# Optimization experiments

Measured on AMD Instinct MI355X. Metric: run time of the kernel, lower is better.

## Reference

```python
import jax, jax.numpy as jnp
import numpy as np

B, T, I, H = 32, 512, 512, 512


def setup_inputs() -> dict:
    key = jax.random.key(0)
    k1, k2, k3, k4, k5 = jax.random.split(key, 5)
    s = 1.0 / np.sqrt(H)
    return {
        "x": jax.random.normal(k1, (B, T, I), dtype=jnp.float32),
        "Wx": jax.random.normal(k2, (4 * H, I), dtype=jnp.float32) * s,
        "bx": jax.random.normal(k3, (4 * H,), dtype=jnp.float32) * s,
        "Wh": jax.random.normal(k4, (4 * H, H), dtype=jnp.float32) * s,
        "bh": jax.random.normal(k5, (4 * H,), dtype=jnp.float32) * s,
    }


def _cell(gx, h, c, Wh, bh):
    # gx: [B, 4H] precomputed x2h contribution (incl. bx)
    gates = gx + h @ Wh.T + bh
    i_g, f_g, g_g, o_g = jnp.split(gates, 4, axis=1)  # torch chunk order
    i_t = jax.nn.sigmoid(i_g)
    f_t = jax.nn.sigmoid(f_g)
    g_t = jnp.tanh(g_g)
    o_t = jax.nn.sigmoid(o_g)
    cy = c * f_t + i_t * g_t
    hy = o_t * jnp.tanh(cy)
    return hy, cy


def reference(x, Wx, bx, Wh, bh):
    b, t, _ = x.shape
    hdim = Wh.shape[1]
    # Precompute input-to-hidden for all timesteps: [T, B, 4H]
    gx = (jnp.einsum('bti,gi->btg', x, Wx) + bx).transpose(1, 0, 2)
    gx_rev = gx[::-1]  # backward direction reads input[:, -t-1, :]

    h0 = jnp.zeros((b, hdim), dtype=x.dtype)
    carry0 = (h0, h0, h0, h0)  # hf, cf, hb, cb

    def step(carry, inp):
        hf, cf, hb, cb = carry
        gxf, gxb = inp
        hf, cf = _cell(gxf, hf, cf, Wh, bh)
        hb, cb = _cell(gxb, hb, cb, Wh, bh)
        return (hf, cf, hb, cb), (hf, hb)

    _, (out_f, out_b) = jax.lax.scan(step, carry0, (gx, gx_rev))
    # Faithful to original: backward outputs stacked in processing order (no flip)
    out = jnp.concatenate([out_f.transpose(1, 0, 2), out_b.transpose(1, 0, 2)], axis=2)
    return out
```

## Files before the change

kernel.cpp:

```cpp
#include <hip/hip_runtime.h>
#include <stdint.h>

typedef unsigned short ushort_t;
typedef float f32x4 __attribute__((ext_vector_type(4)));
typedef short short8 __attribute__((ext_vector_type(8)));

#define B_ 32
#define T_ 512
#define I_ 512
#define H_ 512
#define G_ 2048

__device__ __forceinline__ ushort_t f2bf(float f) {
    uint32_t u = __float_as_uint(f);
    u += 0x7FFFu + ((u >> 16) & 1u);
    return (ushort_t)(u >> 16);
}
__device__ __forceinline__ float bf2f(ushort_t s) {
    return __uint_as_float(((uint32_t)s) << 16);
}
__device__ __forceinline__ float sigm(float x) { return 1.0f / (1.0f + __expf(-x)); }
__device__ __forceinline__ float tanhx(float x) {
    float e = __expf(-2.0f * fabsf(x));
    float t = (1.0f - e) / (1.0f + e);
    return x >= 0.0f ? t : -t;
}

__global__ __launch_bounds__(256) void kcast(const float* __restrict__ in,
                                             ushort_t* __restrict__ out, int n4) {
    int i = blockIdx.x * 256 + threadIdx.x;
    if (i < n4) {
        float4 v = ((const float4*)in)[i];
        ushort4 o;
        o.x = f2bf(v.x); o.y = f2bf(v.y); o.z = f2bf(v.z); o.w = f2bf(v.w);
        ((ushort4*)out)[i] = o;
    }
}

__global__ __launch_bounds__(256) void kbias(const float* __restrict__ bx,
                                             const float* __restrict__ bh,
                                             float* __restrict__ bias) {
    int i = blockIdx.x * 256 + threadIdx.x;
    if (i < G_) bias[i] = bx[i] + bh[i];
}

__global__ __launch_bounds__(256, 2) void kgemm(const ushort_t* __restrict__ A,
                                                const ushort_t* __restrict__ Bm,
                                                const float* __restrict__ bias,
                                                ushort_t* __restrict__ C) {
    __shared__ __align__(16) ushort_t LA[4096];
    __shared__ __align__(16) ushort_t LB[4096];
    const int tid = threadIdx.x;
    const int lane = tid & 63, w = tid >> 6;
    const int quad = lane >> 4, l16 = lane & 15;
    const int bn = blockIdx.x, bm = blockIdx.y;
    const int wr = w >> 1, wc = w & 1;

    f32x4 acc[4][4] = {};

    for (int kt = 0; kt < 16; ++kt) {
#pragma unroll
        for (int r = 0; r < 2; ++r) {
            int o = r * 256 + tid;
            int m = o >> 2, slot = o & 3;
            int kc = slot ^ ((m >> 1) & 3);
            const ushort_t* ga = A  + (size_t)(bm * 128 + m) * I_ + kt * 32 + kc * 8;
            const ushort_t* gb = Bm + (size_t)(bn * 128 + m) * I_ + kt * 32 + kc * 8;
            __builtin_amdgcn_global_load_lds(
                (const __attribute__((address_space(1))) void*)ga,
                (__attribute__((address_space(3))) void*)(&LA[r * 2048 + w * 512]), 16, 0, 0);
            __builtin_amdgcn_global_load_lds(
                (const __attribute__((address_space(1))) void*)gb,
                (__attribute__((address_space(3))) void*)(&LB[r * 2048 + w * 512]), 16, 0, 0);
        }
        __syncthreads();

        short8 av[4], bv[4];
#pragma unroll
        for (int mt = 0; mt < 4; ++mt) {
            int mm = wr * 64 + mt * 16 + l16;
            av[mt] = *(const short8*)&LA[mm * 32 + ((quad ^ ((mm >> 1) & 3)) << 3)];
            int nn = wc * 64 + mt * 16 + l16;
            bv[mt] = *(const short8*)&LB[nn * 32 + ((quad ^ ((nn >> 1) & 3)) << 3)];
        }
#pragma unroll
        for (int mt = 0; mt < 4; ++mt)
#pragma unroll
            for (int nt = 0; nt < 4; ++nt)
                acc[mt][nt] = __builtin_amdgcn_mfma_f32_16x16x32_bf16(av[mt], bv[nt], acc[mt][nt], 0, 0, 0);
        __syncthreads();
    }

#pragma unroll
    for (int nt = 0; nt < 4; ++nt) {
        int n = bn * 128 + wc * 64 + nt * 16 + l16;
        int gate = n >> 9, jj = (n >> 4) & 31, d = n & 15;
        int np = jj * 64 + gate * 16 + d;
        float bvl = bias[n];
#pragma unroll
        for (int mt = 0; mt < 4; ++mt) {
#pragma unroll
            for (int rg = 0; rg < 4; ++rg) {
                int m = bm * 128 + wr * 64 + mt * 16 + quad * 4 + rg;
                C[(size_t)m * G_ + np] = f2bf(acc[mt][nt][rg] + bvl);
            }
        }
    }
}

__global__ __launch_bounds__(256, 1) void krec(const ushort_t* __restrict__ gx,
                                               const ushort_t* __restrict__ whb,
                                               unsigned long long* __restrict__ hgf,
                                               unsigned long long* __restrict__ hga,
                                               uint32_t* __restrict__ xtab,
                                               float* __restrict__ out) {
    __shared__ __align__(16) ushort_t hl[16 * 520];
    __shared__ float gates[4][16][16];
    __shared__ uint32_t sx[256];
    __shared__ int s_grp, s_j, s_pure;
    const int tid = threadIdx.x;
    const int lane = tid & 63, w = tid >> 6;
    const int quad = lane >> 4, l16 = lane & 15;
    const int bk = blockIdx.x;

    for (int t = tid; t < (16 * 520) / 2; t += 256) ((uint32_t*)hl)[t] = 0;

    uint32_t xcd;
    asm("s_getreg_b32 %0, hwreg(HW_REG_XCC_ID)" : "=s"(xcd));
    xcd &= 7u;
    if (tid == 0)
        __hip_atomic_store(&xtab[bk], 0x100u | xcd, __ATOMIC_RELAXED, __HIP_MEMORY_SCOPE_AGENT);
    {
        uint32_t e = 0;
        for (int spin = 0; spin < (1 << 16); ++spin) {
            e = __hip_atomic_load(&xtab[tid], __ATOMIC_RELAXED, __HIP_MEMORY_SCOPE_AGENT);
            if (e & 0x100u) break;
            __builtin_amdgcn_s_sleep(8);
        }
        sx[tid] = e;
    }
    __syncthreads();
    if (tid == 0) {
        int cnt[8] = {0,0,0,0,0,0,0,0};
        int allvalid = 1;
        for (int i = 0; i < 256; ++i) {
            if (!(sx[i] & 0x100u)) allvalid = 0;
            cnt[sx[i] & 7u]++;
        }
        int balanced = allvalid;
        for (int x = 0; x < 8; ++x) if (cnt[x] != 32) balanced = 0;
        int pre[9]; pre[0] = 0;
        for (int x = 0; x < 8; ++x) pre[x + 1] = pre[x] + cnt[x];
        int rank = pre[xcd];
        for (int i = 0; i < bk; ++i) if ((sx[i] & 7u) == xcd) rank++;
        s_grp = rank >> 5; s_j = rank & 31;
        __hip_atomic_store(&xtab[256 + bk], 0x200u | (uint32_t)balanced,
                           __ATOMIC_RELAXED, __HIP_MEMORY_SCOPE_AGENT);
    }
    __syncthreads();
    {
        uint32_t v = 0;
        for (int spin = 0; spin < (1 << 16); ++spin) {
            v = __hip_atomic_load(&xtab[256 + tid], __ATOMIC_RELAXED, __HIP_MEMORY_SCOPE_AGENT);
            if (v & 0x200u) break;
            __builtin_amdgcn_s_sleep(8);
        }
        sx[tid] = (v & 0x200u) ? (v & 1u) : 0u;
    }
    __syncthreads();
    if (tid == 0) {
        int p = 1;
        for (int i = 0; i < 256; ++i) p &= (int)sx[i];
        s_pure = p;
    }
    __syncthreads();
    const int grp = s_grp, j = s_j;
    const bool pure = (s_pure != 0);

    short8 bw[16];
    {
        const ushort_t* wp = whb + (size_t)(w * H_ + j * 16 + l16) * H_ + quad * 8;
#pragma unroll
        for (int kc = 0; kc < 16; ++kc) bw[kc] = *(const short8*)(wp + kc * 32);
    }

    const int r = tid >> 4, d = tid & 15;
    const int rr = r & 7, half = r >> 3;
    const bool cell = (tid < 128);
    const int b = grp * 4 + (r & 3), dir = (r >> 2) & 1;
    float c = 0.0f;

    unsigned long long* hgrpF = hgf + (size_t)grp * 4096;
    unsigned long long* hgrpA = hga + (size_t)grp * 4096;

    const int base0 = rr * 256 + half * 128 + d * 4;

    for (int n = 0; n < 512; ++n) {
        ushort_t g0 = 0, g1 = 0, g2 = 0, g3 = 0;
        if (cell) {
            int te = dir ? (511 - n) : n;
            const ushort_t* gp = gx + (size_t)(b * T_ + te) * G_ + j * 64 + d;
            g0 = gp[0]; g1 = gp[16]; g2 = gp[32]; g3 = gp[48];
        }

        const uint32_t un = (uint32_t)n;
        uint32_t pay[8];

        if (pure) {
            const unsigned long long* f0 = hgrpF + (size_t)(n & 1) * 2048 + base0;
            unsigned long long tv[8];
            for (int spin = 0; spin < 2048; ++spin) {
#pragma unroll
                for (int i = 0; i < 8; ++i)
                    tv[i] = __hip_atomic_load(f0 + (i >> 2) * 64 + (i & 3),
                                              __ATOMIC_RELAXED, __HIP_MEMORY_SCOPE_AGENT);
                bool ok = true;
#pragma unroll
                for (int i = 0; i < 8; ++i)
                    ok &= ((uint32_t)(tv[i] >> 32) >= un);
                if (ok) break;
                __builtin_amdgcn_s_sleep(1);
            }
#pragma unroll
            for (int i = 0; i < 8; ++i) pay[i] = (uint32_t)tv[i];
        } else {
            const unsigned long long* a0 = hgrpA + (size_t)(n & 1) * 2048 + base0;
            unsigned long long tv[8];
            for (int spin = 0; spin < 600; ++spin) {
#pragma unroll
                for (int i = 0; i < 8; ++i)
                    tv[i] = __hip_atomic_load(a0 + (i >> 2) * 64 + (i & 3),
                                              __ATOMIC_RELAXED, __HIP_MEMORY_SCOPE_AGENT);
                bool ok = true;
#pragma unroll
                for (int i = 0; i < 8; ++i)
                    ok &= ((uint32_t)(tv[i] >> 32) >= un);
                if (ok) break;
                __builtin_amdgcn_s_sleep(4);
            }
#pragma unroll
            for (int i = 0; i < 8; ++i) pay[i] = (uint32_t)tv[i];
        }

#pragma unroll
        for (int cc = 0; cc < 2; ++cc) {
            uint4 pk;
            pk.x = pay[cc * 4 + 0];
            pk.y = pay[cc * 4 + 1];
            pk.z = pay[cc * 4 + 2];
            pk.w = pay[cc * 4 + 3];
            *(uint4*)&hl[rr * 520 + half * 256 + cc * 128 + d * 8] = pk;
        }
        __syncthreads();

        f32x4 acc0 = {}, acc1 = {};
#pragma unroll
        for (int kc = 0; kc < 16; kc += 2) {
            short8 av0 = *(const short8*)&hl[l16 * 520 + kc * 32 + quad * 8];
            acc0 = __builtin_amdgcn_mfma_f32_16x16x32_bf16(av0, bw[kc], acc0, 0, 0, 0);
            short8 av1 = *(const short8*)&hl[l16 * 520 + (kc + 1) * 32 + quad * 8];
            acc1 = __builtin_amdgcn_mfma_f32_16x16x32_bf16(av1, bw[kc + 1], acc1, 0, 0, 0);
        }
        f32x4 acc = acc0 + acc1;
#pragma unroll
        for (int rg = 0; rg < 4; ++rg) gates[w][quad * 4 + rg][l16] = acc[rg];
        __syncthreads();

        if (cell) {
            float gi = gates[0][r][d] + bf2f(g0);
            float gf = gates[1][r][d] + bf2f(g1);
            float gg = gates[2][r][d] + bf2f(g2);
            float go = gates[3][r][d] + bf2f(g3);
            float it = sigm(gi), ft = sigm(gf), gt = tanhx(gg), ot = sigm(go);
            c = c * ft + it * gt;
            float h = ot * tanhx(c);

            int hv = (int)f2bf(h);
            int vo = __shfl(hv, lane ^ 1);
            if (!(d & 1)) {
                uint32_t payv = (((uint32_t)vo & 0xFFFFu) << 16) | ((uint32_t)hv & 0xFFFFu);
                size_t u = (size_t)((n + 1) & 1) * 2048 + (size_t)r * 256 + j * 8 + (d >> 1);
                uint2 uv; uv.x = payv; uv.y = (uint32_t)(n + 1);
                asm volatile("global_store_dwordx2 %0, %1, off"
                             :: "v"((void*)(hgrpF + u)), "v"(uv) : "memory");
                if (!pure) {
                    unsigned long long unit =
                        ((unsigned long long)(uint32_t)(n + 1) << 32) | payv;
                    __hip_atomic_store(hgrpA + u, unit,
                                       __ATOMIC_RELAXED, __HIP_MEMORY_SCOPE_AGENT);
                }
            }
            out[(size_t)b * (T_ * 2 * H_) + (size_t)n * (2 * H_) + dir * H_ + j * 16 + d] = h;
        }
    }
}

#define GX_OFF    ((size_t)0)
#define XB_OFF    ((size_t)67108864)
#define HGF_OFF   XB_OFF
#define HGA_OFF   (XB_OFF + 262144)
#define XTAB_OFF  (XB_OFF + 524288)
#define HG_BYTES  ((size_t)(524288 + 2048))
#define WXB_OFF   ((size_t)83886080)
#define WHB_OFF   ((size_t)85983232)
#define BIAS_OFF  ((size_t)88080384)
#define WS_NEED   ((size_t)88088576)

extern "C" void kernel_launch(void* const* d_in, const int* in_sizes, int n_in,
                              void* d_out, int out_size, void* d_ws, size_t ws_size,
                              hipStream_t stream) {
    if (ws_size < WS_NEED) return;

    const float* x  = (const float*)d_in[0];
    const float* Wx = (const float*)d_in[1];
    const float* bx = (const float*)d_in[2];
    const float* Wh = (const float*)d_in[3];
    const float* bh = (const float*)d_in[4];
    float* out = (float*)d_out;
    char* ws = (char*)d_ws;

    ushort_t* gx   = (ushort_t*)(ws + GX_OFF);
    ushort_t* xb   = (ushort_t*)(ws + XB_OFF);
    ushort_t* wxb  = (ushort_t*)(ws + WXB_OFF);
    ushort_t* whb  = (ushort_t*)(ws + WHB_OFF);
    float*    bias = (float*)(ws + BIAS_OFF);
    unsigned long long* hgf = (unsigned long long*)(ws + HGF_OFF);
    unsigned long long* hga = (unsigned long long*)(ws + HGA_OFF);
    uint32_t* xtab = (uint32_t*)(ws + XTAB_OFF);

    kcast<<<dim3((B_ * T_ * I_ / 4 + 255) / 256), 256, 0, stream>>>(x, xb, B_ * T_ * I_ / 4);
    kcast<<<dim3((G_ * I_ / 4 + 255) / 256), 256, 0, stream>>>(Wx, wxb, G_ * I_ / 4);
    kcast<<<dim3((G_ * H_ / 4 + 255) / 256), 256, 0, stream>>>(Wh, whb, G_ * H_ / 4);
    kbias<<<dim3(G_ / 256), 256, 0, stream>>>(bx, bh, bias);

    kgemm<<<dim3(G_ / 128, (B_ * T_) / 128), 256, 0, stream>>>(xb, wxb, bias, gx);

    hipMemsetAsync(ws + HGF_OFF, 0, HG_BYTES, stream);

    krec<<<dim3(256), 256, 0, stream>>>(gx, whb, hgf, hga, xtab, out);
}
```

Before: 1.127 ms.

## Replace per-word sequence tags with per-block done flags in recurrent handoff

In the pure (same-XCD) path, the h-state exchange buffer no longer carries a step counter next to every 32-bit payload word. Each wave now packs four bf16 values per 64-bit store, waits on vmcnt, then publishes a done flag. Consumers spin on a compact 64-entry flag array with one load per lane and a wave vote, then read the packed payload once. This halves exchange traffic and cuts the polling load count. The cost is an extra store-to-flag ordering step, which relies on relaxed stores becoming visible in order.

```diff
diff --git a/kernel.cpp b/kernel.cpp
--- a/kernel.cpp
+++ b/kernel.cpp
@@ -112,6 +112,7 @@
                                                const ushort_t* __restrict__ whb,
                                                unsigned long long* __restrict__ hgf,
                                                unsigned long long* __restrict__ hga,
+                                               unsigned long long* __restrict__ dn,
                                                uint32_t* __restrict__ xtab,
                                                float* __restrict__ out) {
     __shared__ __align__(16) ushort_t hl[16 * 520];
@@ -188,12 +189,16 @@
     const int rr = r & 7, half = r >> 3;
     const bool cell = (tid < 128);
     const int b = grp * 4 + (r & 3), dir = (r >> 2) & 1;
+    const int wv = (r >> 2) & 1 ? 0 : 0;
+    const int cwave = tid >> 6;
     float c = 0.0f;
 
-    unsigned long long* hgrpF = hgf + (size_t)grp * 4096;
+    unsigned long long* hgrpF = hgf + (size_t)grp * 2048;
     unsigned long long* hgrpA = hga + (size_t)grp * 4096;
-
-    const int base0 = rr * 256 + half * 128 + d * 4;
+    unsigned long long* dgrp  = dn  + (size_t)grp * 64;
+
+    const int fbase = rr * 128 + half * 64 + d * 4;
+    const int abase = rr * 256 + half * 128 + d * 4;
 
     for (int n = 0; n < 512; ++n) {
         ushort_t g0 = 0, g1 = 0, g2 = 0, g3 = 0;
@@ -204,27 +209,29 @@
         }
 
         const uint32_t un = (uint32_t)n;
-        uint32_t pay[8];
 
         if (pure) {
-            const unsigned long long* f0 = hgrpF + (size_t)(n & 1) * 2048 + base0;
-            unsigned long long tv[8];
-            for (int spin = 0; spin < 2048; ++spin) {
-#pragma unroll
-                for (int i = 0; i < 8; ++i)
-                    tv[i] = __hip_atomic_load(f0 + (i >> 2) * 64 + (i & 3),
-                                              __ATOMIC_RELAXED, __HIP_MEMORY_SCOPE_AGENT);
-                bool ok = true;
-#pragma unroll
-                for (int i = 0; i < 8; ++i)
-                    ok &= ((uint32_t)(tv[i] >> 32) >= un);
-                if (ok) break;
+            for (int spin = 0; spin < 8192; ++spin) {
+                unsigned long long v = __hip_atomic_load(dgrp + lane, __ATOMIC_RELAXED,
+                                                         __HIP_MEMORY_SCOPE_AGENT);
+                if (__all((uint32_t)v >= un)) break;
                 __builtin_amdgcn_s_sleep(1);
             }
-#pragma unroll
-            for (int i = 0; i < 8; ++i) pay[i] = (uint32_t)tv[i];
+            const unsigned long long* f0 = hgrpF + (size_t)(n & 1) * 1024 + fbase;
+            unsigned long long t0 = __hip_atomic_load(f0 + 0, __ATOMIC_RELAXED, __HIP_MEMORY_SCOPE_AGENT);
+            unsigned long long t1 = __hip_atomic_load(f0 + 1, __ATOMIC_RELAXED, __HIP_MEMORY_SCOPE_AGENT);
+            unsigned long long t2 = __hip_atomic_load(f0 + 2, __ATOMIC_RELAXED, __HIP_MEMORY_SCOPE_AGENT);
+            unsigned long long t3 = __hip_atomic_load(f0 + 3, __ATOMIC_RELAXED, __HIP_MEMORY_SCOPE_AGENT);
+            uint4 p0, p1;
+            p0.x = (uint32_t)t0; p0.y = (uint32_t)(t0 >> 32);
+            p0.z = (uint32_t)t1; p0.w = (uint32_t)(t1 >> 32);
+            p1.x = (uint32_t)t2; p1.y = (uint32_t)(t2 >> 32);
+            p1.z = (uint32_t)t3; p1.w = (uint32_t)(t3 >> 32);
+            int hb = rr * 520 + half * 256 + d * 16;
+            *(uint4*)&hl[hb] = p0;
+            *(uint4*)&hl[hb + 8] = p1;
         } else {
-            const unsigned long long* a0 = hgrpA + (size_t)(n & 1) * 2048 + base0;
+            const unsigned long long* a0 = hgrpA + (size_t)(n & 1) * 2048 + abase;
             unsigned long long tv[8];
             for (int spin = 0; spin < 600; ++spin) {
 #pragma unroll
@@ -239,17 +246,14 @@
                 __builtin_amdgcn_s_sleep(4);
             }
 #pragma unroll
-            for (int i = 0; i < 8; ++i) pay[i] = (uint32_t)tv[i];
-        }
-
-#pragma unroll
-        for (int cc = 0; cc < 2; ++cc) {
-            uint4 pk;
-            pk.x = pay[cc * 4 + 0];
-            pk.y = pay[cc * 4 + 1];
-            pk.z = pay[cc * 4 + 2];
-            pk.w = pay[cc * 4 + 3];
-            *(uint4*)&hl[rr * 520 + half * 256 + cc * 128 + d * 8] = pk;
+            for (int cc = 0; cc < 2; ++cc) {
+                uint4 pk;
+                pk.x = (uint32_t)tv[cc * 4 + 0];
+                pk.y = (uint32_t)tv[cc * 4 + 1];
+                pk.z = (uint32_t)tv[cc * 4 + 2];
+                pk.w = (uint32_t)tv[cc * 4 + 3];
+                *(uint4*)&hl[rr * 520 + half * 256 + cc * 128 + d * 8] = pk;
+            }
         }
         __syncthreads();
 
@@ -276,16 +280,33 @@
             float h = ot * tanhx(c);
 
             int hv = (int)f2bf(h);
-            int vo = __shfl(hv, lane ^ 1);
-            if (!(d & 1)) {
-                uint32_t payv = (((uint32_t)vo & 0xFFFFu) << 16) | ((uint32_t)hv & 0xFFFFu);
-                size_t u = (size_t)((n + 1) & 1) * 2048 + (size_t)r * 256 + j * 8 + (d >> 1);
-                uint2 uv; uv.x = payv; uv.y = (uint32_t)(n + 1);
-                asm volatile("global_store_dwordx2 %0, %1, off"
-                             :: "v"((void*)(hgrpF + u)), "v"(uv) : "memory");
-                if (!pure) {
+            if (pure) {
+                int v1 = __shfl(hv, lane + 1);
+                int v2 = __shfl(hv, lane + 2);
+                int v3 = __shfl(hv, lane + 3);
+                if (!(d & 3)) {
+                    uint2 uv;
+                    uv.x = ((uint32_t)hv & 0xFFFFu) | ((uint32_t)v1 << 16);
+                    uv.y = ((uint32_t)v2 & 0xFFFFu) | ((uint32_t)v3 << 16);
+                    unsigned long long* fp = hgrpF + (size_t)((n + 1) & 1) * 1024
+                                           + (size_t)r * 128 + j * 4 + (d >> 2);
+                    asm volatile("global_store_dwordx2 %0, %1, off"
+                                 :: "v"((void*)fp), "v"(uv) : "memory");
+                }
+                asm volatile("s_waitcnt vmcnt(0)");
+                if (lane == 0) {
+                    uint2 dv; dv.x = (uint32_t)(n + 1); dv.y = 0;
+                    unsigned long long* dp = dgrp + (size_t)j * 2 + cwave;
+                    asm volatile("global_store_dwordx2 %0, %1, off"
+                                 :: "v"((void*)dp), "v"(dv) : "memory");
+                }
+            } else {
+                int vo = __shfl(hv, lane ^ 1);
+                if (!(d & 1)) {
+                    uint32_t payv = (((uint32_t)vo & 0xFFFFu) << 16) | ((uint32_t)hv & 0xFFFFu);
                     unsigned long long unit =
                         ((unsigned long long)(uint32_t)(n + 1) << 32) | payv;
+                    size_t u = (size_t)((n + 1) & 1) * 2048 + (size_t)r * 256 + j * 8 + (d >> 1);
                     __hip_atomic_store(hgrpA + u, unit,
                                        __ATOMIC_RELAXED, __HIP_MEMORY_SCOPE_AGENT);
                 }
@@ -298,9 +319,10 @@
 #define GX_OFF    ((size_t)0)
 #define XB_OFF    ((size_t)67108864)
 #define HGF_OFF   XB_OFF
-#define HGA_OFF   (XB_OFF + 262144)
-#define XTAB_OFF  (XB_OFF + 524288)
-#define HG_BYTES  ((size_t)(524288 + 2048))
+#define HGA_OFF   (XB_OFF + 131072)
+#define DONE_OFF  (XB_OFF + 393216)
+#define XTAB_OFF  (XB_OFF + 397312)
+#define HG_BYTES  ((size_t)(397312 + 2048))
 #define WXB_OFF   ((size_t)83886080)
 #define WHB_OFF   ((size_t)85983232)
 #define BIAS_OFF  ((size_t)88080384)
@@ -326,6 +348,7 @@
     float*    bias = (float*)(ws + BIAS_OFF);
     unsigned long long* hgf = (unsigned long long*)(ws + HGF_OFF);
     unsigned long long* hga = (unsigned long long*)(ws + HGA_OFF);
+    unsigned long long* dn  = (unsigned long long*)(ws + DONE_OFF);
     uint32_t* xtab = (uint32_t*)(ws + XTAB_OFF);
 
     kcast<<<dim3((B_ * T_ * I_ / 4 + 255) / 256), 256, 0, stream>>>(x, xb, B_ * T_ * I_ / 4);
@@ -337,5 +360,5 @@
 
     hipMemsetAsync(ws + HGF_OFF, 0, HG_BYTES, stream);
 
-    krec<<<dim3(256), 256, 0, stream>>>(gx, whb, hgf, hga, xtab, out);
-}
+    krec<<<dim3(256), 256, 0, stream>>>(gx, whb, hgf, hga, dn, xtab, out);
+}
```

After: 954.3 us. 15.3% less time.
